# Performance work log

Hardware: AMD Instinct MI355X
Metric: run time of the kernel (lower is better)

The kernel has to match this reference:

```python
import jax, jax.numpy as jnp
import numpy as np

EPS = 1e-08


def squash(s):
    # s: [B, out_caps, out_d]
    s2 = jnp.sum(s * s, axis=-1, keepdims=True)
    return s2 / (1.0 + s2) * (s / jnp.sqrt(s2 + EPS))


def setup_inputs() -> dict:
    key = jax.random.key(0)
    k1, k2 = jax.random.split(key)
    B, in_caps, out_caps, in_d, out_d = 128, 1152, 32, 8, 16
    u = jax.random.normal(k1, (B, in_caps, in_d), dtype=jnp.float32)
    weight = jax.random.normal(k2, (in_caps, out_caps, in_d, out_d), dtype=jnp.float32)
    return {"u": u, "weight": weight, "iterations": 3}


def reference(u, weight, iterations):
    # u: [B, in_caps, in_d]; weight: [in_caps, out_caps, in_d, out_d]
    u_hat = jnp.einsum('ijnm,bin->bijm', weight, u)  # [B, i, j, m]
    B, in_caps, out_caps, _ = u_hat.shape
    b = jnp.zeros((B, in_caps, out_caps), dtype=u.dtype)
    v = None
    for _ in range(iterations):
        c = jax.nn.softmax(b, axis=1)  # faithful to torch code: softmax over in_caps
        s = jnp.einsum('bij,bijm->bjm', c, u_hat)
        v = squash(s)
        a = jnp.einsum('bjm,bijm->bij', v, u_hat)
        b = b + a
    return v
```

## Files before the change

### kernel.cpp

```cpp
#include <hip/hip_runtime.h>
#include <stdint.h>

constexpr int B_SZ     = 128;
constexpr int IN_CAPS  = 1152;
constexpr int OUT_CAPS = 32;
constexpr int IN_D     = 8;
constexpr int OUT_D    = 16;
constexpr int ITERS    = 3;

constexpr int THREADS  = 1024;
constexpr int NW       = THREADS / 64;
constexpr int G        = 2;
constexpr int TILE_R   = 128;
constexpr int NTILE    = IN_CAPS / TILE_R;
constexpr int ROW_F    = 128;

typedef const uint32_t __attribute__((address_space(1)))* gptr_t;
typedef uint32_t       __attribute__((address_space(3)))* lptr_t;
__device__ __forceinline__ void async_copy16(const float* g, float* l) {
    __builtin_amdgcn_global_load_lds((gptr_t)g, (lptr_t)l, 16, 0, 0);
}

__global__ __launch_bounds__(THREADS) void caps_route(
    const float* __restrict__ u,
    const float* __restrict__ w,
    float* __restrict__ out)
{
    __shared__ __align__(16) float tile[2][TILE_R * ROW_F];
    __shared__ float red_es[NW * 8];
    __shared__ __align__(16) float red_m[NW * 8 * 4];

    const int nwg = gridDim.x;
    const int bid = blockIdx.x;
    const int wid = (bid & 7) * (nwg >> 3) + (bid >> 3);
    const int j   = wid >> 6;
    const int b0  = (wid & 63) * G;

    const int tid  = threadIdx.x;
    const int lane = tid & 63;
    const int wv   = tid >> 6;
    const int bl   = tid & 1;
    const int mq   = (tid >> 1) & 3;
    const int ir   = tid >> 3;
    const int b    = b0 + bl;

    const int mir = (ir & 7) | ((ir & 3) << 3);
    int foff[8];
    #pragma unroll
    for (int n = 0; n < 8; ++n) foff[n] = (((4 * n + mq) ^ mir) << 2);

    float uh[NTILE][4];
    float4 uA0, uA1, uB0, uB1;

    #define STAGE_TILE(NB, T)                                                 \
    do {                                                                      \
        _Pragma("unroll")                                                     \
        for (int q = 0; q < 4; ++q) {                                         \
            const int Lb   = (wv * 4 + q) * 64;      \
            const int L    = Lb + lane;                                       \
            const int row  = L >> 5;                                          \
            const int slot = L & 31;                                          \
            const int c    = slot ^ ((row & 7) | ((row & 3) << 3));           \
            const float* gsrc = w +                                           \
                ((size_t)(((T) * TILE_R + row) * OUT_CAPS + j) * ROW_F + c * 4); \
            async_copy16(gsrc, &tile[(NB)][Lb * 4]);                          \
        }                                                                     \
    } while (0)

    #define COMP_TILE(NB, T, UC0, UC1)                                        \
    do {                                                                      \
        const float* trow = &tile[(NB)][ir * ROW_F];                          \
        const float uc[8] = {UC0.x, UC0.y, UC0.z, UC0.w,                      \
                             UC1.x, UC1.y, UC1.z, UC1.w};                     \
        float4 acc = make_float4(0.f, 0.f, 0.f, 0.f);                         \
        _Pragma("unroll")                                                     \
        for (int n = 0; n < 8; ++n) {                                         \
            const float4 w4 = *reinterpret_cast<const float4*>(trow + foff[n]); \
            acc.x = fmaf(uc[n], w4.x, acc.x);                                 \
            acc.y = fmaf(uc[n], w4.y, acc.y);                                 \
            acc.z = fmaf(uc[n], w4.z, acc.z);                                 \
            acc.w = fmaf(uc[n], w4.w, acc.w);                                 \
        }                                                                     \
        uh[(T)][0] = acc.x; uh[(T)][1] = acc.y;                               \
        uh[(T)][2] = acc.z; uh[(T)][3] = acc.w;                               \
    } while (0)

    #define STEP(T, UC0, UC1, UN0, UN1)                                       \
    do {                                                                      \
        if ((T) + 1 < NTILE) {                                                \
            STAGE_TILE(((T) + 1) & 1, (T) + 1);                               \
            const float* up = u +                                             \
                ((size_t)b * IN_CAPS + ((T) + 1) * TILE_R + ir) * IN_D;       \
            UN0 = *reinterpret_cast<const float4*>(up);                       \
            UN1 = *reinterpret_cast<const float4*>(up + 4);                   \
        }                                                                     \
        COMP_TILE((T) & 1, T, UC0, UC1);                                      \
        __syncthreads();                                                      \
    } while (0)

    STAGE_TILE(0, 0);
    {
        const float* up = u + ((size_t)b * IN_CAPS + ir) * IN_D;
        uA0 = *reinterpret_cast<const float4*>(up);
        uA1 = *reinterpret_cast<const float4*>(up + 4);
    }
    __syncthreads();

    STEP(0, uA0, uA1, uB0, uB1);
    STEP(1, uB0, uB1, uA0, uA1);
    STEP(2, uA0, uA1, uB0, uB1);
    STEP(3, uB0, uB1, uA0, uA1);
    STEP(4, uA0, uA1, uB0, uB1);
    STEP(5, uB0, uB1, uA0, uA1);
    STEP(6, uA0, uA1, uB0, uB1);
    STEP(7, uB0, uB1, uA0, uA1);
    STEP(8, uA0, uA1, uB0, uB1);
    #undef STEP
    #undef COMP_TILE
    #undef STAGE_TILE

    float blog[NTILE];
    #pragma unroll
    for (int r = 0; r < NTILE; ++r) blog[r] = 0.0f;
    float vv[4];
    const int grp = lane & 7;

    for (int it = 0; it < ITERS; ++it) {
        float e[NTILE];
        float esum = 0.0f;
        #pragma unroll
        for (int r = 0; r < NTILE; ++r) { e[r] = __expf(blog[r]); esum += e[r]; }
        esum += __shfl_xor(esum, 8);
        esum += __shfl_xor(esum, 16);
        esum += __shfl_xor(esum, 32);

        float sp0 = 0.f, sp1 = 0.f, sp2 = 0.f, sp3 = 0.f;
        #pragma unroll
        for (int r = 0; r < NTILE; ++r) {
            sp0 = fmaf(e[r], uh[r][0], sp0);
            sp1 = fmaf(e[r], uh[r][1], sp1);
            sp2 = fmaf(e[r], uh[r][2], sp2);
            sp3 = fmaf(e[r], uh[r][3], sp3);
        }
        sp0 += __shfl_xor(sp0, 8);  sp1 += __shfl_xor(sp1, 8);
        sp2 += __shfl_xor(sp2, 8);  sp3 += __shfl_xor(sp3, 8);
        sp0 += __shfl_xor(sp0, 16); sp1 += __shfl_xor(sp1, 16);
        sp2 += __shfl_xor(sp2, 16); sp3 += __shfl_xor(sp3, 16);
        sp0 += __shfl_xor(sp0, 32); sp1 += __shfl_xor(sp1, 32);
        sp2 += __shfl_xor(sp2, 32); sp3 += __shfl_xor(sp3, 32);

        if (lane < 8) {
            red_es[wv * 8 + lane] = esum;
            *reinterpret_cast<float4*>(&red_m[(wv * 8 + lane) * 4]) =
                make_float4(sp0, sp1, sp2, sp3);
        }
        __syncthreads();
        float gsum = 0.0f;
        float sa0 = 0.f, sa1 = 0.f, sa2 = 0.f, sa3 = 0.f;
        #pragma unroll
        for (int q = 0; q < NW; ++q) {
            gsum += red_es[q * 8 + grp];
            const float4 rm =
                *reinterpret_cast<const float4*>(&red_m[(q * 8 + grp) * 4]);
            sa0 += rm.x; sa1 += rm.y; sa2 += rm.z; sa3 += rm.w;
        }
        __syncthreads();

        const float cinv = 1.0f / gsum;
        vv[0] = sa0 * cinv; vv[1] = sa1 * cinv;
        vv[2] = sa2 * cinv; vv[3] = sa3 * cinv;
        float s2 = fmaf(vv[0], vv[0], fmaf(vv[1], vv[1],
                   fmaf(vv[2], vv[2], vv[3] * vv[3])));
        s2 += __shfl_xor(s2, 2);
        s2 += __shfl_xor(s2, 4);
        const float scale = (s2 / (1.0f + s2)) * rsqrtf(s2 + 1e-8f);
        vv[0] *= scale; vv[1] *= scale; vv[2] *= scale; vv[3] *= scale;

        if (it < ITERS - 1) {
            #pragma unroll
            for (int r = 0; r < NTILE; ++r) {
                float a = fmaf(vv[0], uh[r][0], fmaf(vv[1], uh[r][1],
                          fmaf(vv[2], uh[r][2], vv[3] * uh[r][3])));
                a += __shfl_xor(a, 2);
                a += __shfl_xor(a, 4);
                blog[r] += a;
            }
        }
    }

    if (tid < 8) {
        float4* op = reinterpret_cast<float4*>(
            out + ((size_t)(b0 + bl) * OUT_CAPS + j) * OUT_D + mq * 4);
        *op = make_float4(vv[0], vv[1], vv[2], vv[3]);
    }
}

extern "C" void kernel_launch(void* const* d_in, const int* in_sizes, int n_in,
                              void* d_out, int out_size, void* d_ws, size_t ws_size,
                              hipStream_t stream) {
    const float* u = (const float*)d_in[0];
    const float* w = (const float*)d_in[1];
    float* out     = (float*)d_out;
    (void)in_sizes; (void)n_in; (void)out_size; (void)d_ws; (void)ws_size;

    dim3 grid(OUT_CAPS * (B_SZ / G));
    dim3 block(THREADS);
    hipLaunchKernelGGL(caps_route, grid, block, 0, stream, u, w, out);
}
```

Before: 158.0 us.

## Single-buffer weight tile in LDS and keep routing logits as exponentials

Replaces the double-buffered LDS weight tile with a single buffer, which halves shared memory per block and may allow more resident blocks. Loading the next tile now waits behind two barriers per step, so global loads no longer overlap with compute. The XOR swizzle is simplified so each row needs two base offsets instead of eight precomputed ones, reducing register use. Routing now keeps exp(b) directly and multiplies by exp(a) each iteration instead of re-exponentiating accumulated logits, which could overflow if logits grow large.

```diff
diff --git a/kernel.cpp b/kernel.cpp
--- a/kernel.cpp
+++ b/kernel.cpp
@@ -26,7 +26,7 @@
     const float* __restrict__ w,
     float* __restrict__ out)
 {
-    __shared__ __align__(16) float tile[2][TILE_R * ROW_F];
+    __shared__ __align__(16) float tile[TILE_R * ROW_F];
     __shared__ float red_es[NW * 8];
     __shared__ __align__(16) float red_m[NW * 8 * 4];
 
@@ -44,15 +44,14 @@
     const int ir   = tid >> 3;
     const int b    = b0 + bl;
 
-    const int mir = (ir & 7) | ((ir & 3) << 3);
-    int foff[8];
-    #pragma unroll
-    for (int n = 0; n < 8; ++n) foff[n] = (((4 * n + mq) ^ mir) << 2);
+    const int pmir = (ir & 7) ^ ((ir & 1) << 2);
+    const int o0   = ((mq ^ pmir) << 2);
+    const int o1   = (((4 | mq) ^ pmir) << 2);
 
     float uh[NTILE][4];
-    float4 uA0, uA1, uB0, uB1;
-
-    #define STAGE_TILE(NB, T)                                                 \
+    float4 uA0, uA1;
+
+    #define STAGE_TILE(T)                                                     \
     do {                                                                      \
         _Pragma("unroll")                                                     \
         for (int q = 0; q < 4; ++q) {                                         \
@@ -60,76 +59,73 @@
             const int L    = Lb + lane;                                       \
             const int row  = L >> 5;                                          \
             const int slot = L & 31;                                          \
-            const int c    = slot ^ ((row & 7) | ((row & 3) << 3));           \
+            const int c    = slot ^ ((row & 7) ^ ((row & 1) << 2));           \
             const float* gsrc = w +                                           \
                 ((size_t)(((T) * TILE_R + row) * OUT_CAPS + j) * ROW_F + c * 4); \
-            async_copy16(gsrc, &tile[(NB)][Lb * 4]);                          \
+            async_copy16(gsrc, &tile[Lb * 4]);                                \
         }                                                                     \
     } while (0)
 
-    #define COMP_TILE(NB, T, UC0, UC1)                                        \
-    do {                                                                      \
-        const float* trow = &tile[(NB)][ir * ROW_F];                          \
-        const float uc[8] = {UC0.x, UC0.y, UC0.z, UC0.w,                      \
-                             UC1.x, UC1.y, UC1.z, UC1.w};                     \
+    #define ULOAD(T)                                                          \
+    do {                                                                      \
+        const float* up = u + ((size_t)b * IN_CAPS + (T) * TILE_R + ir) * IN_D; \
+        uA0 = *reinterpret_cast<const float4*>(up);                           \
+        uA1 = *reinterpret_cast<const float4*>(up + 4);                       \
+    } while (0)
+
+    #define COMP_TILE(T)                                                      \
+    do {                                                                      \
+        const float* trow = &tile[ir * ROW_F];                                \
+        const float uc[8] = {uA0.x, uA0.y, uA0.z, uA0.w,                      \
+                             uA1.x, uA1.y, uA1.z, uA1.w};                     \
         float4 acc = make_float4(0.f, 0.f, 0.f, 0.f);                         \
         _Pragma("unroll")                                                     \
-        for (int n = 0; n < 8; ++n) {                                         \
-            const float4 w4 = *reinterpret_cast<const float4*>(trow + foff[n]); \
-            acc.x = fmaf(uc[n], w4.x, acc.x);                                 \
-            acc.y = fmaf(uc[n], w4.y, acc.y);                                 \
-            acc.z = fmaf(uc[n], w4.z, acc.z);                                 \
-            acc.w = fmaf(uc[n], w4.w, acc.w);                                 \
+        for (int t = 0; t < 4; ++t) {                                         \
+            const float4 wa = *reinterpret_cast<const float4*>(trow + t * 32 + o0); \
+            const float4 wb = *reinterpret_cast<const float4*>(trow + t * 32 + o1); \
+            acc.x = fmaf(uc[2*t], wa.x, acc.x);                               \
+            acc.y = fmaf(uc[2*t], wa.y, acc.y);                               \
+            acc.z = fmaf(uc[2*t], wa.z, acc.z);                               \
+            acc.w = fmaf(uc[2*t], wa.w, acc.w);                               \
+            acc.x = fmaf(uc[2*t+1], wb.x, acc.x);                             \
+            acc.y = fmaf(uc[2*t+1], wb.y, acc.y);                             \
+            acc.z = fmaf(uc[2*t+1], wb.z, acc.z);                             \
+            acc.w = fmaf(uc[2*t+1], wb.w, acc.w);                             \
         }                                                                     \
         uh[(T)][0] = acc.x; uh[(T)][1] = acc.y;                               \
         uh[(T)][2] = acc.z; uh[(T)][3] = acc.w;                               \
     } while (0)
 
-    #define STEP(T, UC0, UC1, UN0, UN1)                                       \
-    do {                                                                      \
-        if ((T) + 1 < NTILE) {                                                \
-            STAGE_TILE(((T) + 1) & 1, (T) + 1);                               \
-            const float* up = u +                                             \
-                ((size_t)b * IN_CAPS + ((T) + 1) * TILE_R + ir) * IN_D;       \
-            UN0 = *reinterpret_cast<const float4*>(up);                       \
-            UN1 = *reinterpret_cast<const float4*>(up + 4);                   \
-        }                                                                     \
-        COMP_TILE((T) & 1, T, UC0, UC1);                                      \
+    #define STEP(T)                                                           \
+    do {                                                                      \
         __syncthreads();                                                      \
-    } while (0)
-
-    STAGE_TILE(0, 0);
-    {
-        const float* up = u + ((size_t)b * IN_CAPS + ir) * IN_D;
-        uA0 = *reinterpret_cast<const float4*>(up);
-        uA1 = *reinterpret_cast<const float4*>(up + 4);
-    }
+        STAGE_TILE(T);                                                        \
+        ULOAD(T);                                                             \
+        __syncthreads();                                                      \
+        COMP_TILE(T);                                                         \
+    } while (0)
+
+    STAGE_TILE(0);
+    ULOAD(0);
     __syncthreads();
-
-    STEP(0, uA0, uA1, uB0, uB1);
-    STEP(1, uB0, uB1, uA0, uA1);
-    STEP(2, uA0, uA1, uB0, uB1);
-    STEP(3, uB0, uB1, uA0, uA1);
-    STEP(4, uA0, uA1, uB0, uB1);
-    STEP(5, uB0, uB1, uA0, uA1);
-    STEP(6, uA0, uA1, uB0, uB1);
-    STEP(7, uB0, uB1, uA0, uA1);
-    STEP(8, uA0, uA1, uB0, uB1);
+    COMP_TILE(0);
+    STEP(1); STEP(2); STEP(3); STEP(4);
+    STEP(5); STEP(6); STEP(7); STEP(8);
     #undef STEP
     #undef COMP_TILE
+    #undef ULOAD
     #undef STAGE_TILE
 
-    float blog[NTILE];
+    float e[NTILE];
     #pragma unroll
-    for (int r = 0; r < NTILE; ++r) blog[r] = 0.0f;
+    for (int r = 0; r < NTILE; ++r) e[r] = 1.0f;
     float vv[4];
     const int grp = lane & 7;
 
     for (int it = 0; it < ITERS; ++it) {
-        float e[NTILE];
         float esum = 0.0f;
         #pragma unroll
-        for (int r = 0; r < NTILE; ++r) { e[r] = __expf(blog[r]); esum += e[r]; }
+        for (int r = 0; r < NTILE; ++r) esum += e[r];
         esum += __shfl_xor(esum, 8);
         esum += __shfl_xor(esum, 16);
         esum += __shfl_xor(esum, 32);
@@ -183,7 +179,7 @@
                           fmaf(vv[2], uh[r][2], vv[3] * uh[r][3])));
                 a += __shfl_xor(a, 2);
                 a += __shfl_xor(a, 4);
-                blog[r] += a;
+                e[r] *= __expf(a);
             }
         }
     }
```

New measurement: 175.0 us. 10.8% more time.
